# Optimization experiments

Hardware: AMD Instinct MI355X
Metric: run time of the kernel (lower is better)

Reference implementation:

```python
import jax, jax.numpy as jnp
import numpy as np

D_MODEL = 1024
D_K = 128
SEQ = 4096
NEG = -10000000000.0

def setup_inputs() -> dict:
    key = jax.random.key(0)
    ks = jax.random.split(key, 9)
    q = jax.random.normal(ks[0], (SEQ, D_MODEL), dtype=jnp.float32)
    k = jax.random.normal(ks[1], (SEQ, D_MODEL), dtype=jnp.float32)
    v = jax.random.normal(ks[2], (SEQ, D_MODEL), dtype=jnp.float32)
    s = 1.0 / np.sqrt(D_MODEL)
    Wq = jax.random.normal(ks[3], (D_MODEL, D_K), dtype=jnp.float32) * s
    Wk = jax.random.normal(ks[4], (D_MODEL, D_K), dtype=jnp.float32) * s
    Wv = jax.random.normal(ks[5], (D_MODEL, D_K), dtype=jnp.float32) * s
    bq = jax.random.normal(ks[6], (D_K,), dtype=jnp.float32) * 0.01
    bk = jax.random.normal(ks[7], (D_K,), dtype=jnp.float32) * 0.01
    bv = jax.random.normal(ks[8], (D_K,), dtype=jnp.float32) * 0.01
    return {"q": q, "k": k, "v": v, "Wq": Wq, "bq": bq, "Wk": Wk, "bk": bk, "Wv": Wv, "bv": bv}

def reference(q, k, v, Wq, bq, Wk, bk, Wv, bv):
    # projections (nn.Linear: x @ W + b)
    qp = q @ Wq + bq          # [S, D_k]
    kp = k @ Wk + bk          # [S, D_k]
    vp = v @ Wv + bv          # [S, D_k]
    scores = (qp @ kp.T) / jnp.sqrt(jnp.float32(D_K))  # [S, S]
    S = scores.shape[0]
    causal = jnp.tril(jnp.ones((S, scores.shape[1]), dtype=bool))
    scores = jnp.where(causal, scores, jnp.float32(NEG))
    attn = jax.nn.softmax(scores, axis=-1)
    return attn @ vp          # [S, D_k]
```

## Files before the change

kernel.cpp:

```cpp
#include <hip/hip_runtime.h>
#include <hip/hip_bf16.h>

#define S   4096
#define DM  1024
#define DK  128

typedef __attribute__((ext_vector_type(8))) short short8;
typedef __attribute__((ext_vector_type(4))) float f32x4;

static __device__ __forceinline__ unsigned short f2bf(float f) {
    unsigned u = __builtin_bit_cast(unsigned, f);
    unsigned r = (u + 0x7FFFu + ((u >> 16) & 1u)) >> 16;
    return (unsigned short)r;
}

__global__ __launch_bounds__(256) void wtrans_kernel(
    const float* __restrict__ Wq, const float* __restrict__ Wk,
    const float* __restrict__ Wv, unsigned short* __restrict__ WtB)
{
    const int pid = blockIdx.z;
    const float* W = pid == 0 ? Wq : (pid == 1 ? Wk : Wv);
    unsigned short* T = WtB + (size_t)pid * DK * DM;
    const int k0 = blockIdx.x * 32, c0 = blockIdx.y * 32;
    __shared__ unsigned short tile[32][33];
    const int x = threadIdx.x & 31, y = threadIdx.x >> 5;
    #pragma unroll
    for (int i = 0; i < 32; i += 8)
        tile[y + i][x] = f2bf(W[(size_t)(k0 + y + i) * DK + c0 + x]);
    __syncthreads();
    #pragma unroll
    for (int i = 0; i < 32; i += 8)
        T[(size_t)(c0 + y + i) * DM + k0 + x] = tile[x][y + i];
}

#define PBK 64
__global__ __launch_bounds__(256) void proj_kernel(
    const float* __restrict__ q, const float* __restrict__ k, const float* __restrict__ v,
    const float* __restrict__ bq, const float* __restrict__ bk, const float* __restrict__ bv,
    const unsigned short* __restrict__ WtB,
    unsigned short* __restrict__ qp, unsigned short* __restrict__ kp,
    unsigned short* __restrict__ vpF)
{
    const int pid = blockIdx.y;
    const float* X    = pid == 0 ? q  : (pid == 1 ? k  : v);
    const float* bias = pid == 0 ? bq : (pid == 1 ? bk : bv);
    unsigned short* out = pid == 0 ? qp : (pid == 1 ? kp : vpF);
    const unsigned short* Wt = WtB + (size_t)pid * DK * DM;

    const int rows0 = blockIdx.x * 32;
    const int tid  = threadIdx.x;
    const int lane = tid & 63;
    const int wave = tid >> 6;
    const int lw = lane & 15, lg = lane >> 4;
    const int wrow = (wave >> 1) * 16;
    const int wcol = (wave & 1) * 64;

    __shared__ unsigned short Xs[32][PBK];

    f32x4 acc[4];
    #pragma unroll
    for (int i = 0; i < 4; i++) acc[i] = f32x4{0.f, 0.f, 0.f, 0.f};

    const int srow = tid >> 3;
    const int sg   = tid & 7;
    const int sgs  = sg ^ (srow & 7);

    for (int k0 = 0; k0 < DM; k0 += PBK) {
        const float* src = X + (size_t)(rows0 + srow) * DM + k0 + sg * 8;
        float4 a = *reinterpret_cast<const float4*>(src);
        float4 b = *reinterpret_cast<const float4*>(src + 4);
        short8 xb;
        xb[0] = (short)f2bf(a.x); xb[1] = (short)f2bf(a.y);
        xb[2] = (short)f2bf(a.z); xb[3] = (short)f2bf(a.w);
        xb[4] = (short)f2bf(b.x); xb[5] = (short)f2bf(b.y);
        xb[6] = (short)f2bf(b.z); xb[7] = (short)f2bf(b.w);
        *reinterpret_cast<short8*>(&Xs[srow][sgs * 8]) = xb;
        __syncthreads();
        #pragma unroll
        for (int kk = 0; kk < 2; kk++) {
            const int g = (kk * 4 + lg) ^ (lw & 7);
            short8 af = *reinterpret_cast<const short8*>(&Xs[wrow + lw][g * 8]);
            #pragma unroll
            for (int f = 0; f < 4; f++) {
                const unsigned short* wp =
                    Wt + (size_t)(wcol + f * 16 + lw) * DM + k0 + kk * 32 + lg * 8;
                short8 bf = *reinterpret_cast<const short8*>(wp);
                acc[f] = __builtin_amdgcn_mfma_f32_16x16x32_bf16(af, bf, acc[f], 0, 0, 0);
            }
        }
        __syncthreads();
    }

    const int orow = rows0 + wrow + lg * 4;
    if (pid != 2) {
        #pragma unroll
        for (int f = 0; f < 4; f++) {
            int col = wcol + f * 16 + lw;
            float bb = bias[col];
            #pragma unroll
            for (int r = 0; r < 4; r++)
                out[(size_t)(orow + r) * DK + col] = f2bf(acc[f][r] + bb);
        }
    } else {
        #pragma unroll
        for (int f = 0; f < 4; f++) {
            int col = wcol + f * 16 + lw;
            float bb = bias[col];
            #pragma unroll
            for (int r = 0; r < 4; r++) {
                int row = orow + r;
                out[(size_t)(row >> 5) * DK * 32 + (size_t)col * 32 + (row & 31)] =
                    f2bf(acc[f][r] + bb);
            }
        }
    }
}

__global__ __launch_bounds__(512) void attn_kernel(
    const unsigned short* __restrict__ qp,
    const unsigned short* __restrict__ kp,
    const unsigned short* __restrict__ vpF,
    float* __restrict__ out)
{
    const int tid  = threadIdx.x;
    const int lane = tid & 63;
    const int wid  = tid >> 6;
    const int q0   = blockIdx.x * 16;
    const int lw = lane & 15, lg = lane >> 4;

    __shared__ unsigned short Pl[8][16][32];
    __shared__ float Ols[8][16][132];
    __shared__ float mls[8][16], lls[8][16];
    __shared__ float wgt[8][16], invd[16];

    short8 qf[4];
    {
        const unsigned short* qb = qp + (size_t)(q0 + lw) * DK + lg * 8;
        #pragma unroll
        for (int t = 0; t < 4; t++)
            qf[t] = *reinterpret_cast<const short8*>(qb + t * 32);
    }

    f32x4 oacc[8];
    #pragma unroll
    for (int i = 0; i < 8; i++) oacc[i] = f32x4{0.f, 0.f, 0.f, 0.f};
    float m[4]    = {-1e30f, -1e30f, -1e30f, -1e30f};
    float lsum[4] = {0.f, 0.f, 0.f, 0.f};

    const float scale = 0.08838834764831843f;
    const int nt = (q0 + 47) >> 5;

    for (int t = wid; t < nt; t += 8) {
        const int k0 = t * 32;
        f32x4 sc0 = f32x4{0.f, 0.f, 0.f, 0.f};
        f32x4 sc1 = f32x4{0.f, 0.f, 0.f, 0.f};
        {
            const unsigned short* kb0 = kp + (size_t)(k0 + lw) * DK + lg * 8;
            const unsigned short* kb1 = kb0 + 16 * DK;
            #pragma unroll
            for (int tt = 0; tt < 4; tt++) {
                short8 b0 = *reinterpret_cast<const short8*>(kb0 + tt * 32);
                short8 b1 = *reinterpret_cast<const short8*>(kb1 + tt * 32);
                sc0 = __builtin_amdgcn_mfma_f32_16x16x32_bf16(qf[tt], b0, sc0, 0, 0, 0);
                sc1 = __builtin_amdgcn_mfma_f32_16x16x32_bf16(qf[tt], b1, sc1, 0, 0, 0);
            }
        }
        float mx[4];
        #pragma unroll
        for (int r = 0; r < 4; r++) {
            int qg = q0 + lg * 4 + r;
            float s0 = sc0[r] * scale; if (k0 + lw > qg)      s0 = -1e30f;
            float s1 = sc1[r] * scale; if (k0 + 16 + lw > qg) s1 = -1e30f;
            sc0[r] = s0; sc1[r] = s1;
            mx[r] = fmaxf(s0, s1);
        }
        #pragma unroll
        for (int off = 1; off < 16; off <<= 1) {
            #pragma unroll
            for (int r = 0; r < 4; r++)
                mx[r] = fmaxf(mx[r], __shfl_xor(mx[r], off));
        }
        float corr[4], rs[4];
        #pragma unroll
        for (int r = 0; r < 4; r++) {
            float mn = fmaxf(m[r], mx[r]);
            corr[r] = __expf(m[r] - mn);
            m[r] = mn;
            float p0 = __expf(sc0[r] - mn);
            float p1 = __expf(sc1[r] - mn);
            rs[r] = p0 + p1;
            Pl[wid][lg * 4 + r][lw]      = f2bf(p0);
            Pl[wid][lg * 4 + r][16 + lw] = f2bf(p1);
        }
        #pragma unroll
        for (int off = 1; off < 16; off <<= 1) {
            #pragma unroll
            for (int r = 0; r < 4; r++)
                rs[r] += __shfl_xor(rs[r], off);
        }
        #pragma unroll
        for (int r = 0; r < 4; r++) lsum[r] = lsum[r] * corr[r] + rs[r];
        #pragma unroll
        for (int f = 0; f < 8; f++) {
            oacc[f][0] *= corr[0]; oacc[f][1] *= corr[1];
            oacc[f][2] *= corr[2]; oacc[f][3] *= corr[3];
        }
        asm volatile("s_waitcnt lgkmcnt(0)" ::: "memory");
        short8 pa = *reinterpret_cast<const short8*>(&Pl[wid][lw][lg * 8]);
        const unsigned short* vb = vpF + (size_t)(k0 >> 5) * DK * 32 + lg * 8;
        #pragma unroll
        for (int f = 0; f < 8; f++) {
            short8 bf = *reinterpret_cast<const short8*>(vb + (size_t)(f * 16 + lw) * 32);
            oacc[f] = __builtin_amdgcn_mfma_f32_16x16x32_bf16(pa, bf, oacc[f], 0, 0, 0);
        }
    }

    #pragma unroll
    for (int f = 0; f < 8; f++) {
        int col = f * 16 + lw;
        #pragma unroll
        for (int r = 0; r < 4; r++)
            Ols[wid][lg * 4 + r][col] = oacc[f][r];
    }
    if (lw == 0) {
        #pragma unroll
        for (int r = 0; r < 4; r++) {
            mls[wid][lg * 4 + r] = m[r];
            lls[wid][lg * 4 + r] = lsum[r];
        }
    }
    __syncthreads();

    if (tid < 16) {
        float M = mls[0][tid];
        #pragma unroll
        for (int w2 = 1; w2 < 8; w2++) M = fmaxf(M, mls[w2][tid]);
        float d = 0.f;
        #pragma unroll
        for (int w2 = 0; w2 < 8; w2++) {
            float g = __expf(mls[w2][tid] - M);
            wgt[w2][tid] = g;
            d += g * lls[w2][tid];
        }
        invd[tid] = 1.0f / d;
    }
    __syncthreads();

    #pragma unroll
    for (int j = 0; j < 4; j++) {
        int e = tid + 512 * j;
        int r = e >> 7, c = e & 127;
        float num = 0.f;
        #pragma unroll
        for (int w2 = 0; w2 < 8; w2++) num += wgt[w2][r] * Ols[w2][r][c];
        out[(size_t)(q0 + r) * DK + c] = num * invd[r];
    }
}

extern "C" void kernel_launch(void* const* d_in, const int* in_sizes, int n_in,
                              void* d_out, int out_size, void* d_ws, size_t ws_size,
                              hipStream_t stream) {
    const float* q  = (const float*)d_in[0];
    const float* k  = (const float*)d_in[1];
    const float* v  = (const float*)d_in[2];
    const float* Wq = (const float*)d_in[3];
    const float* bq = (const float*)d_in[4];
    const float* Wk = (const float*)d_in[5];
    const float* bk = (const float*)d_in[6];
    const float* Wv = (const float*)d_in[7];
    const float* bv = (const float*)d_in[8];

    unsigned short* qp  = (unsigned short*)d_ws;
    unsigned short* kp  = qp + (size_t)S * DK;
    unsigned short* vpF = kp + (size_t)S * DK;
    unsigned short* WtB = vpF + (size_t)S * DK;

    dim3 gt(DM / 32, DK / 32, 3);
    wtrans_kernel<<<gt, 256, 0, stream>>>(Wq, Wk, Wv, WtB);

    dim3 gp(S / 32, 3);
    proj_kernel<<<gp, 256, 0, stream>>>(q, k, v, bq, bk, bv, WtB, qp, kp, vpF);

    attn_kernel<<<S / 16, 512, 0, stream>>>(qp, kp, vpF, (float*)d_out);
}
```

Baseline: 174.6 us.

## Split causal attention into per-key-block partial kernels plus a combine pass

Replaces the single attention kernel, which used 512 threads per 16-query block, with a split-K scheme. Each 64-thread block handles one 256-key chunk of one query tile and writes partial O, max and sum to workspace. A second kernel merges the partials with log-sum-exp weighting. The softmax scale is folded into the Q projection. This is meant to balance causal work across many small blocks, at the cost of extra global traffic for fp32 partials and one more launch. It falls back to the old kernel if the workspace is too small.

```diff
diff --git a/kernel.cpp b/kernel.cpp
--- a/kernel.cpp
+++ b/kernel.cpp
@@ -46,6 +46,7 @@
     const float* bias = pid == 0 ? bq : (pid == 1 ? bk : bv);
     unsigned short* out = pid == 0 ? qp : (pid == 1 ? kp : vpF);
     const unsigned short* Wt = WtB + (size_t)pid * DK * DM;
+    const float oscale = pid == 0 ? 0.08838834764831843f : 1.0f;
 
     const int rows0 = blockIdx.x * 32;
     const int tid  = threadIdx.x;
@@ -99,7 +100,7 @@
             float bb = bias[col];
             #pragma unroll
             for (int r = 0; r < 4; r++)
-                out[(size_t)(orow + r) * DK + col] = f2bf(acc[f][r] + bb);
+                out[(size_t)(orow + r) * DK + col] = f2bf((acc[f][r] + bb) * oscale);
         }
     } else {
         #pragma unroll
@@ -116,7 +117,163 @@
     }
 }
 
-__global__ __launch_bounds__(512) void attn_kernel(
+__global__ __launch_bounds__(64) void attn_part_kernel(
+    const unsigned short* __restrict__ qp,
+    const unsigned short* __restrict__ kp,
+    const unsigned short* __restrict__ vpF,
+    float* __restrict__ part_O, float* __restrict__ part_ml)
+{
+    const int i  = blockIdx.y;
+    const int kb = blockIdx.x;
+    const int nkb = (i + 16) >> 4;
+    if (kb >= nkb) return;
+    const int a = i >> 4, rr = i & 15;
+    const int u = 8 * a * (a + 1) + rr * (a + 1) + kb;
+
+    const int lane = threadIdx.x;
+    const int lw = lane & 15, lg = lane >> 4;
+    const int q0 = i * 16;
+    const int kstart = kb * 256;
+    const int kend = min(kstart + 256, q0 + 16);
+    const int ntl = (kend - kstart + 31) >> 5;
+
+    __shared__ unsigned short Pl[16][32];
+
+    short8 qf[4];
+    {
+        const unsigned short* qb = qp + (size_t)(q0 + lw) * DK + lg * 8;
+        #pragma unroll
+        for (int t = 0; t < 4; t++)
+            qf[t] = *reinterpret_cast<const short8*>(qb + t * 32);
+    }
+
+    f32x4 oacc[8];
+    #pragma unroll
+    for (int i2 = 0; i2 < 8; i2++) oacc[i2] = f32x4{0.f, 0.f, 0.f, 0.f};
+    float m[4]    = {-1e30f, -1e30f, -1e30f, -1e30f};
+    float lsum[4] = {0.f, 0.f, 0.f, 0.f};
+
+    for (int t = 0; t < ntl; ++t) {
+        const int k0 = kstart + t * 32;
+        f32x4 sc0 = f32x4{0.f, 0.f, 0.f, 0.f};
+        f32x4 sc1 = f32x4{0.f, 0.f, 0.f, 0.f};
+        {
+            const unsigned short* kb0 = kp + (size_t)(k0 + lw) * DK + lg * 8;
+            const unsigned short* kb1 = kb0 + 16 * DK;
+            #pragma unroll
+            for (int tt = 0; tt < 4; tt++) {
+                short8 b0 = *reinterpret_cast<const short8*>(kb0 + tt * 32);
+                short8 b1 = *reinterpret_cast<const short8*>(kb1 + tt * 32);
+                sc0 = __builtin_amdgcn_mfma_f32_16x16x32_bf16(qf[tt], b0, sc0, 0, 0, 0);
+                sc1 = __builtin_amdgcn_mfma_f32_16x16x32_bf16(qf[tt], b1, sc1, 0, 0, 0);
+            }
+        }
+        float mx[4];
+        #pragma unroll
+        for (int r = 0; r < 4; r++) {
+            int qg = q0 + lg * 4 + r;
+            float s0 = sc0[r]; if (k0 + lw > qg)      s0 = -1e30f;
+            float s1 = sc1[r]; if (k0 + 16 + lw > qg) s1 = -1e30f;
+            sc0[r] = s0; sc1[r] = s1;
+            mx[r] = fmaxf(s0, s1);
+        }
+        #pragma unroll
+        for (int off = 1; off < 16; off <<= 1) {
+            #pragma unroll
+            for (int r = 0; r < 4; r++)
+                mx[r] = fmaxf(mx[r], __shfl_xor(mx[r], off));
+        }
+        float corr[4], rs[4];
+        #pragma unroll
+        for (int r = 0; r < 4; r++) {
+            float mn = fmaxf(m[r], mx[r]);
+            corr[r] = __expf(m[r] - mn);
+            m[r] = mn;
+            float p0 = __expf(sc0[r] - mn);
+            float p1 = __expf(sc1[r] - mn);
+            rs[r] = p0 + p1;
+            Pl[lg * 4 + r][lw]      = f2bf(p0);
+            Pl[lg * 4 + r][16 + lw] = f2bf(p1);
+        }
+        #pragma unroll
+        for (int off = 1; off < 16; off <<= 1) {
+            #pragma unroll
+            for (int r = 0; r < 4; r++)
+                rs[r] += __shfl_xor(rs[r], off);
+        }
+        #pragma unroll
+        for (int r = 0; r < 4; r++) lsum[r] = lsum[r] * corr[r] + rs[r];
+        #pragma unroll
+        for (int f = 0; f < 8; f++) {
+            oacc[f][0] *= corr[0]; oacc[f][1] *= corr[1];
+            oacc[f][2] *= corr[2]; oacc[f][3] *= corr[3];
+        }
+        asm volatile("s_waitcnt lgkmcnt(0)" ::: "memory");
+        short8 pa = *reinterpret_cast<const short8*>(&Pl[lw][lg * 8]);
+        const unsigned short* vb = vpF + (size_t)(k0 >> 5) * DK * 32 + lg * 8;
+        #pragma unroll
+        for (int f = 0; f < 8; f++) {
+            short8 bf = *reinterpret_cast<const short8*>(vb + (size_t)(f * 16 + lw) * 32);
+            oacc[f] = __builtin_amdgcn_mfma_f32_16x16x32_bf16(pa, bf, oacc[f], 0, 0, 0);
+        }
+    }
+
+    float* po = part_O + (size_t)u * 2048;
+    #pragma unroll
+    for (int f = 0; f < 8; f++) {
+        int col = f * 16 + lw;
+        #pragma unroll
+        for (int r = 0; r < 4; r++)
+            po[(lg * 4 + r) * DK + col] = oacc[f][r];
+    }
+    if (lw == 0) {
+        #pragma unroll
+        for (int r = 0; r < 4; r++) {
+            part_ml[(size_t)u * 32 + lg * 4 + r]      = m[r];
+            part_ml[(size_t)u * 32 + 16 + lg * 4 + r] = lsum[r];
+        }
+    }
+}
+
+__global__ __launch_bounds__(128) void attn_comb_kernel(
+    const float* __restrict__ part_O, const float* __restrict__ part_ml,
+    float* __restrict__ out)
+{
+    const int i = blockIdx.x;
+    const int nkb = (i + 16) >> 4;
+    const int a = i >> 4, rr = i & 15;
+    const int u0 = 8 * a * (a + 1) + rr * (a + 1);
+    const int tid = threadIdx.x;
+
+    __shared__ float wgt[16][16];
+    __shared__ float invd[16];
+
+    if (tid < 16) {
+        float M = -1e30f;
+        for (int u = 0; u < nkb; u++)
+            M = fmaxf(M, part_ml[(size_t)(u0 + u) * 32 + tid]);
+        float d = 0.f;
+        for (int u = 0; u < nkb; u++) {
+            float g = __expf(part_ml[(size_t)(u0 + u) * 32 + tid] - M);
+            wgt[u][tid] = g;
+            d += g * part_ml[(size_t)(u0 + u) * 32 + 16 + tid];
+        }
+        invd[tid] = 1.0f / d;
+    }
+    __syncthreads();
+
+    #pragma unroll
+    for (int j = 0; j < 16; j++) {
+        int e = tid + 128 * j;
+        int r = e >> 7;
+        float acc = 0.f;
+        for (int u = 0; u < nkb; u++)
+            acc += wgt[u][r] * part_O[(size_t)(u0 + u) * 2048 + e];
+        out[(size_t)i * 2048 + e] = acc * invd[r];
+    }
+}
+
+__global__ __launch_bounds__(512) void attn_fallback_kernel(
     const unsigned short* __restrict__ qp,
     const unsigned short* __restrict__ kp,
     const unsigned short* __restrict__ vpF,
@@ -140,14 +297,11 @@
         for (int t = 0; t < 4; t++)
             qf[t] = *reinterpret_cast<const short8*>(qb + t * 32);
     }
-
     f32x4 oacc[8];
     #pragma unroll
     for (int i = 0; i < 8; i++) oacc[i] = f32x4{0.f, 0.f, 0.f, 0.f};
     float m[4]    = {-1e30f, -1e30f, -1e30f, -1e30f};
     float lsum[4] = {0.f, 0.f, 0.f, 0.f};
-
-    const float scale = 0.08838834764831843f;
     const int nt = (q0 + 47) >> 5;
 
     for (int t = wid; t < nt; t += 8) {
@@ -169,8 +323,8 @@
         #pragma unroll
         for (int r = 0; r < 4; r++) {
             int qg = q0 + lg * 4 + r;
-            float s0 = sc0[r] * scale; if (k0 + lw > qg)      s0 = -1e30f;
-            float s1 = sc1[r] * scale; if (k0 + 16 + lw > qg) s1 = -1e30f;
+            float s0 = sc0[r]; if (k0 + lw > qg)      s0 = -1e30f;
+            float s1 = sc1[r]; if (k0 + 16 + lw > qg) s1 = -1e30f;
             sc0[r] = s0; sc1[r] = s1;
             mx[r] = fmaxf(s0, s1);
         }
@@ -214,7 +368,6 @@
             oacc[f] = __builtin_amdgcn_mfma_f32_16x16x32_bf16(pa, bf, oacc[f], 0, 0, 0);
         }
     }
-
     #pragma unroll
     for (int f = 0; f < 8; f++) {
         int col = f * 16 + lw;
@@ -230,7 +383,6 @@
         }
     }
     __syncthreads();
-
     if (tid < 16) {
         float M = mls[0][tid];
         #pragma unroll
@@ -245,7 +397,6 @@
         invd[tid] = 1.0f / d;
     }
     __syncthreads();
-
     #pragma unroll
     for (int j = 0; j < 4; j++) {
         int e = tid + 512 * j;
@@ -274,6 +425,11 @@
     unsigned short* kp  = qp + (size_t)S * DK;
     unsigned short* vpF = kp + (size_t)S * DK;
     unsigned short* WtB = vpF + (size_t)S * DK;
+    float* part_O  = (float*)(WtB + (size_t)3 * DK * DM);
+    float* part_ml = part_O + (size_t)2176 * 2048;
+
+    const size_t ws_need = ((size_t)3 * S * DK + (size_t)3 * DK * DM) * 2 +
+                           ((size_t)2176 * 2048 + (size_t)2176 * 32) * 4;
 
     dim3 gt(DM / 32, DK / 32, 3);
     wtrans_kernel<<<gt, 256, 0, stream>>>(Wq, Wk, Wv, WtB);
@@ -281,5 +437,11 @@
     dim3 gp(S / 32, 3);
     proj_kernel<<<gp, 256, 0, stream>>>(q, k, v, bq, bk, bv, WtB, qp, kp, vpF);
 
-    attn_kernel<<<S / 16, 512, 0, stream>>>(qp, kp, vpF, (float*)d_out);
-}
+    if (ws_size >= ws_need) {
+        dim3 ga(16, S / 16);
+        attn_part_kernel<<<ga, 64, 0, stream>>>(qp, kp, vpF, part_O, part_ml);
+        attn_comb_kernel<<<S / 16, 128, 0, stream>>>(part_O, part_ml, (float*)d_out);
+    } else {
+        attn_fallback_kernel<<<S / 16, 512, 0, stream>>>(qp, kp, vpF, (float*)d_out);
+    }
+}
```

Result: slower. 217.3 us (+24.5%).
